# Kernel optimization log

Measured on AMD Instinct MI355X. Metric: run time of the kernel, lower is better.

Reference implementation:

```python
import jax, jax.numpy as jnp
import numpy as np

F_, E_, B_, D_, H_, O_ = 4, 8, 4096, 512, 1024, 512


def setup_inputs() -> dict:
    key = jax.random.key(0)
    ks = jax.random.split(key, 7)
    s = 0.02  # small init scale to keep activations sane
    return {
        "features": jax.random.normal(ks[0], (F_, B_, D_), jnp.float32),
        "W1": jax.random.normal(ks[1], (F_, E_, D_, H_), jnp.float32) * s,
        "b1": jax.random.normal(ks[2], (F_, E_, H_), jnp.float32) * s,
        "W2": jax.random.normal(ks[3], (F_, E_, H_, O_), jnp.float32) * s,
        "b2": jax.random.normal(ks[4], (F_, E_, O_), jnp.float32) * s,
        "Wg": jax.random.normal(ks[5], (F_, D_, E_), jnp.float32) * s,
        "bg": jax.random.normal(ks[6], (F_, E_), jnp.float32) * s,
    }


def reference(features, W1, b1, W2, b2, Wg, bg):
    # Gate: softmax over experts, per feature. [F,B,E]
    gate = jax.nn.softmax(jnp.einsum('fbd,fde->fbe', features, Wg) + bg[:, None, :], axis=-1)
    # All experts computed densely (soft MoE): hidden [F,B,E,H]
    h = jax.nn.relu(jnp.einsum('fbd,fedh->fbeh', features, W1) + b1[:, None, :, :])
    # Expert outputs [F,B,E,O]
    eo = jnp.einsum('fbeh,feho->fbeo', h, W2) + b2[:, None, :, :]
    # Gate-weighted sum over experts, then mean over features -> [B,O]
    weighted = jnp.einsum('fbe,fbeo->fbo', gate, eo)
    return jnp.mean(weighted, axis=0)
```

## Files before the change

kernel.cpp:

```cpp
#include <hip/hip_runtime.h>


#define F_ 4
#define E_ 8
#define B_ 4096
#define D_ 512
#define H_ 1024
#define O_ 512

typedef unsigned short ushort_t;
typedef __bf16 bf16x8 __attribute__((ext_vector_type(8)));
typedef float f32x4 __attribute__((ext_vector_type(4)));
typedef unsigned short ushort8_t __attribute__((ext_vector_type(8)));

__device__ inline ushort_t f2bf(float f) {
  union { float f; unsigned u; } v; v.f = f;
  unsigned r = v.u + 0x7FFFu + ((v.u >> 16) & 1u);
  return (ushort_t)(r >> 16);
}
__device__ inline float bf2f(ushort_t u) {
  union { unsigned u; float f; } v; v.u = ((unsigned)u) << 16;
  return v.f;
}

__device__ inline void async16(const void* g, void* l) {
  __builtin_amdgcn_global_load_lds(
      (const __attribute__((address_space(1))) unsigned int*)g,
      (__attribute__((address_space(3))) unsigned int*)l, 16, 0, 0);
}

__device__ inline unsigned ldsOff(const void* p) {
  return (unsigned)(unsigned long long)(const __attribute__((address_space(3))) char*)p;
}
__device__ inline bf16x8 dsr128(unsigned byteOff) {
  bf16x8 r;
  asm volatile("ds_read_b128 %0, %1" : "=v"(r) : "v"(byteOff));
  return r;
}

__global__ void prep_kernel(const float* __restrict__ features, const float* __restrict__ Wg,
                            const float* __restrict__ bg, float* __restrict__ g2,
                            ushort_t* __restrict__ featbf) {
  const int fb = blockIdx.x;
  const int f = fb >> 12, b = fb & (B_ - 1);
  const int lane = threadIdx.x;
  const float* feat = features + ((size_t)f * B_ + b) * D_;
  const float* wg = Wg + (size_t)f * D_ * E_;
  const int d0 = lane * 8;
  float ff[8];
  *(float4*)&ff[0] = *(const float4*)&feat[d0];
  *(float4*)&ff[4] = *(const float4*)&feat[d0 + 4];
  ushort8_t u;
#pragma unroll
  for (int k = 0; k < 8; ++k) u[k] = f2bf(ff[k]);
  *(ushort8_t*)&featbf[((size_t)f * B_ + b) * D_ + d0] = u;

  float acc[E_] = {0.f, 0.f, 0.f, 0.f, 0.f, 0.f, 0.f, 0.f};
#pragma unroll
  for (int k = 0; k < 8; ++k) {
    const float fv = ff[k];
    const float4 w0 = ((const float4*)(wg + (size_t)(d0 + k) * E_))[0];
    const float4 w1 = ((const float4*)(wg + (size_t)(d0 + k) * E_))[1];
    acc[0] += fv * w0.x; acc[1] += fv * w0.y; acc[2] += fv * w0.z; acc[3] += fv * w0.w;
    acc[4] += fv * w1.x; acc[5] += fv * w1.y; acc[6] += fv * w1.z; acc[7] += fv * w1.w;
  }
#pragma unroll
  for (int off = 32; off >= 1; off >>= 1)
#pragma unroll
    for (int e = 0; e < E_; ++e) acc[e] += __shfl_xor(acc[e], off, 64);
  float lg[E_], mx = -1e30f;
#pragma unroll
  for (int e = 0; e < E_; ++e) { lg[e] = acc[e] + bg[f * E_ + e]; mx = fmaxf(mx, lg[e]); }
  float s = 0.f;
#pragma unroll
  for (int e = 0; e < E_; ++e) { lg[e] = __expf(lg[e] - mx); s += lg[e]; }
  const float inv = 1.f / (s * (float)F_);
  if (lane < E_) g2[((size_t)f * B_ + b) * E_ + lane] = lg[lane] * inv;
}

__global__ void transpose_cast_kernel(const float* __restrict__ in, ushort_t* __restrict__ out,
                                      int R, int C) {
  __shared__ float tile[64][65];
  const size_t zoff = (size_t)blockIdx.z * R * C;
  in += zoff; out += zoff;
  const int tx = threadIdx.x & 63, ty = threadIdx.x >> 6;
  const int r0 = blockIdx.y * 64, c0 = blockIdx.x * 64;
#pragma unroll
  for (int i = 0; i < 16; ++i) {
    const int r = ty + i * 4;
    tile[r][tx] = in[(size_t)(r0 + r) * C + c0 + tx];
  }
  __syncthreads();
#pragma unroll
  for (int i = 0; i < 16; ++i) {
    const int c = ty + i * 4;
    out[(size_t)(c0 + c) * R + r0 + tx] = f2bf(tile[tx][c]);
  }
}


#define FSW(r) (((r) + ((r) >> 2)) & 3)

#define VM8 asm volatile("s_waitcnt vmcnt(8)" ::: "memory")
#define VM4 asm volatile("s_waitcnt vmcnt(4)" ::: "memory")
#define VM0 asm volatile("s_waitcnt vmcnt(0)" ::: "memory")
#define VMN ((void)0)

#define G1_STAGE(ktn, SLOT) { \
    ushort_t* s_ = &lds[(SLOT) * 8192]; \
    const ushort_t* a_ = aG + (ktn) * 32; \
    const ushort_t* b_ = bG + (ktn) * 32; \
    async16(a_,           s_ + t * 8); \
    async16(a_ + 64 * D_, s_ + 2048 + t * 8); \
    async16(b_,           s_ + 4096 + t * 8); \
    async16(b_ + 64 * D_, s_ + 6144 + t * 8); }

#define G2_STAGE(ktn, SLOT) { \
    ushort_t* s_ = &lds[(SLOT) * 8192]; \
    const ushort_t* a_ = HfA + (size_t)((ktn) >> 5) * ((size_t)B_ * H_) + aOff + ((ktn) & 31) * 32; \
    const ushort_t* b_ = w2A + (size_t)((ktn) >> 5) * ((size_t)O_ * H_) + bOff + ((ktn) & 31) * 32; \
    async16(a_,           s_ + t * 8); \
    async16(a_ + 64 * H_, s_ + 2048 + t * 8); \
    async16(b_,           s_ + 4096 + t * 8); \
    async16(b_ + 64 * H_, s_ + 6144 + t * 8); }

#define GSTEP(kt, SLOT, STG, VMS, STAGEM) { \
    const unsigned sb = ldsB + (SLOT) * 16384u; \
    bf16x8 af[4], bfr[4]; \
    _Pragma("unroll") for (int i_ = 0; i_ < 4; ++i_) af[i_] = dsr128(sb + aRd + i_ * 1024u); \
    _Pragma("unroll") for (int j_ = 0; j_ < 4; ++j_) bfr[j_] = dsr128(sb + bRd + j_ * 1024u); \
    asm volatile("s_waitcnt lgkmcnt(0)" ::: "memory"); \
    __builtin_amdgcn_sched_barrier(0); \
    __builtin_amdgcn_s_setprio(1); \
    _Pragma("unroll") for (int i_ = 0; i_ < 4; ++i_) \
      _Pragma("unroll") for (int j_ = 0; j_ < 4; ++j_) \
        acc[i_][j_] = __builtin_amdgcn_mfma_f32_16x16x32_bf16(bfr[j_], af[i_], acc[i_][j_], 0, 0, 0); \
    __builtin_amdgcn_s_setprio(0); \
    __builtin_amdgcn_sched_barrier(0); \
    __builtin_amdgcn_s_barrier(); \
    if (STG) { STAGEM((kt) + 3, SLOT); } \
    VMS; \
    __builtin_amdgcn_s_barrier(); \
    __builtin_amdgcn_sched_barrier(0); }

__global__ __launch_bounds__(256, 3) void gemm1_kernel(
    const ushort_t* __restrict__ featbf, const ushort_t* __restrict__ w1t,
    const float* __restrict__ b1, const float* __restrict__ g2,
    ushort_t* __restrict__ Hf, int f) {
  __shared__ __align__(16) ushort_t lds[24576];
  const int id = blockIdx.x;
  const int e = id & 7;
  const int s = id >> 3;
  const int n0 = (s & 7) * 128;
  const int m0 = (s >> 3) * 128;
  const ushort_t* A  = featbf + (size_t)f * B_ * D_;
  const ushort_t* Bp = w1t + ((size_t)f * E_ + e) * (size_t)H_ * D_;
  const float* b1e = b1 + ((size_t)f * E_ + e) * H_;
  const float* g2f = g2 + (size_t)f * B_ * E_;
  ushort_t* HfE = Hf + (size_t)e * B_ * H_;

  const int t = threadIdx.x, lane = t & 63, w = t >> 6;
  const int wm = w & 1, wn = w >> 1;
  const int lr = lane & 15, q = lane >> 4;
  const unsigned ldsB = ldsOff(lds);
  const unsigned caBy = (unsigned)((q ^ FSW(lr)) * 16);
  const unsigned aRd = (unsigned)((wm * 64 + lr) * 64) + caBy;
  const unsigned bRd = 8192u + (unsigned)((wn * 64 + lr) * 64) + caBy;

  const int rr = t >> 2;
  const int cc = (t & 3) ^ FSW(rr);
  const ushort_t* aG = A  + (size_t)(m0 + rr) * D_ + cc * 8;
  const ushort_t* bG = Bp + (size_t)(n0 + rr) * D_ + cc * 8;

  f32x4 acc[4][4];
#pragma unroll
  for (int i = 0; i < 4; ++i)
#pragma unroll
    for (int j = 0; j < 4; ++j) acc[i][j] = (f32x4){0.f, 0.f, 0.f, 0.f};

  G1_STAGE(0, 0); G1_STAGE(1, 1); G1_STAGE(2, 2);
  VM8;
  __builtin_amdgcn_s_barrier();
  __builtin_amdgcn_sched_barrier(0);

  for (int b = 0; b < 12; b += 3) {
    GSTEP(b + 0, 0, 1, VM8, G1_STAGE);
    GSTEP(b + 1, 1, 1, VM8, G1_STAGE);
    GSTEP(b + 2, 2, 1, VM8, G1_STAGE);
  }
  GSTEP(12, 0, 1, VM8, G1_STAGE);
  GSTEP(13, 1, 0, VM4, G1_STAGE);
  GSTEP(14, 2, 0, VM0, G1_STAGE);
  GSTEP(15, 0, 0, VMN, G1_STAGE);

  ushort_t* cb = lds;
#pragma unroll
  for (int i = 0; i < 4; ++i) {
    const int ml = wm * 64 + i * 16 + lr;
    const float gv = g2f[(size_t)(m0 + ml) * E_ + e];
#pragma unroll
    for (int j = 0; j < 4; ++j) {
      const int nl = wn * 64 + j * 16 + q * 4;
      const float4 bb = *(const float4*)&b1e[n0 + nl];
      ushort4 o;
      o.x = f2bf(fmaxf(acc[i][j][0] + bb.x, 0.f) * gv);
      o.y = f2bf(fmaxf(acc[i][j][1] + bb.y, 0.f) * gv);
      o.z = f2bf(fmaxf(acc[i][j][2] + bb.z, 0.f) * gv);
      o.w = f2bf(fmaxf(acc[i][j][3] + bb.w, 0.f) * gv);
      *(ushort4*)&cb[ml * 136 + nl] = o;
    }
  }
  __syncthreads();
  const int row = t >> 1, half = t & 1;
  const ushort_t* src = &cb[row * 136 + half * 64];
  ushort_t* dst = HfE + (size_t)(m0 + row) * H_ + n0 + half * 64;
#pragma unroll
  for (int c = 0; c < 8; ++c)
    *(ushort8_t*)(dst + c * 8) = *(const ushort8_t*)(src + c * 8);
}

__global__ __launch_bounds__(256, 3) void gemm2_kernel(
    const ushort_t* __restrict__ Hf, const ushort_t* __restrict__ w2t,
    const float* __restrict__ b2, const float* __restrict__ g2,
    ushort_t* __restrict__ part, int f) {
  __shared__ __align__(16) ushort_t lds[24576];
  const int id = blockIdx.x;
  const int grp = id & 3;
  const int s = id >> 2;
  const int n0 = (s & 3) * 128;
  const int m0 = (s >> 2) * 128;
  const int e0 = grp * 2;
  const ushort_t* HfA = Hf + (size_t)e0 * B_ * H_;
  const ushort_t* w2A = w2t + ((size_t)f * E_ + e0) * (size_t)O_ * H_;
  const float* g2f = g2 + (size_t)f * B_ * E_;

  const int t = threadIdx.x, lane = t & 63, w = t >> 6;
  const int wm = w & 1, wn = w >> 1;
  const int lr = lane & 15, q = lane >> 4;
  const unsigned ldsB = ldsOff(lds);
  const unsigned caBy = (unsigned)((q ^ FSW(lr)) * 16);
  const unsigned aRd = (unsigned)((wm * 64 + lr) * 64) + caBy;
  const unsigned bRd = 8192u + (unsigned)((wn * 64 + lr) * 64) + caBy;

  const int rr = t >> 2;
  const int cc = (t & 3) ^ FSW(rr);
  const size_t aOff = (size_t)(m0 + rr) * H_ + cc * 8;
  const size_t bOff = (size_t)(n0 + rr) * H_ + cc * 8;

  f32x4 acc[4][4];
#pragma unroll
  for (int i = 0; i < 4; ++i)
#pragma unroll
    for (int j = 0; j < 4; ++j) acc[i][j] = (f32x4){0.f, 0.f, 0.f, 0.f};

  G2_STAGE(0, 0); G2_STAGE(1, 1); G2_STAGE(2, 2);
  VM8;
  __builtin_amdgcn_s_barrier();
  __builtin_amdgcn_sched_barrier(0);

  for (int b = 0; b < 60; b += 3) {
    GSTEP(b + 0, 0, 1, VM8, G2_STAGE);
    GSTEP(b + 1, 1, 1, VM8, G2_STAGE);
    GSTEP(b + 2, 2, 1, VM8, G2_STAGE);
  }
  GSTEP(60, 0, 1, VM8, G2_STAGE);
  GSTEP(61, 1, 0, VM4, G2_STAGE);
  GSTEP(62, 2, 0, VM0, G2_STAGE);
  GSTEP(63, 0, 0, VMN, G2_STAGE);

  ushort_t* cb = lds;
  const float* b2e0 = b2 + ((size_t)f * E_ + e0) * O_;
  const float* b2e1 = b2e0 + O_;
#pragma unroll
  for (int i = 0; i < 4; ++i) {
    const int ml = wm * 64 + i * 16 + lr;
    const float gv0 = g2f[(size_t)(m0 + ml) * E_ + e0];
    const float gv1 = g2f[(size_t)(m0 + ml) * E_ + e0 + 1];
#pragma unroll
    for (int j = 0; j < 4; ++j) {
      const int nl = wn * 64 + j * 16 + q * 4;
      const int n = n0 + nl;
      const float4 c0 = *(const float4*)&b2e0[n];
      const float4 c1 = *(const float4*)&b2e1[n];
      ushort4 o;
      o.x = f2bf(acc[i][j][0] + gv0 * c0.x + gv1 * c1.x);
      o.y = f2bf(acc[i][j][1] + gv0 * c0.y + gv1 * c1.y);
      o.z = f2bf(acc[i][j][2] + gv0 * c0.z + gv1 * c1.z);
      o.w = f2bf(acc[i][j][3] + gv0 * c0.w + gv1 * c1.w);
      *(ushort4*)&cb[ml * 136 + nl] = o;
    }
  }
  __syncthreads();
  const int row = t >> 1, half = t & 1;
  const ushort_t* src = &cb[row * 136 + half * 64];
  ushort_t* dst = part + (size_t)(f * 4 + grp) * (B_ * O_) + (size_t)(m0 + row) * O_ + n0 + half * 64;
#pragma unroll
  for (int c = 0; c < 8; ++c)
    *(ushort8_t*)(dst + c * 8) = *(const ushort8_t*)(src + c * 8);
}

__global__ void reduce_kernel(const ushort_t* __restrict__ part, float* __restrict__ out) {
  const size_t p = ((size_t)blockIdx.x * 256 + threadIdx.x) * 8;
  float s[8] = {0.f, 0.f, 0.f, 0.f, 0.f, 0.f, 0.f, 0.f};
#pragma unroll
  for (int k = 0; k < F_ * 4; ++k) {
    const ushort8_t u = *(const ushort8_t*)&part[(size_t)k * (B_ * O_) + p];
#pragma unroll
    for (int j = 0; j < 8; ++j) s[j] += bf2f(u[j]);
  }
  float4 o0 = {s[0], s[1], s[2], s[3]}, o1 = {s[4], s[5], s[6], s[7]};
  *(float4*)&out[p] = o0;
  *(float4*)&out[p + 4] = o1;
}

extern "C" void kernel_launch(void* const* d_in, const int* in_sizes, int n_in,
                              void* d_out, int out_size, void* d_ws, size_t ws_size,
                              hipStream_t stream) {
  const float* features = (const float*)d_in[0];
  const float* W1 = (const float*)d_in[1];
  const float* b1 = (const float*)d_in[2];
  const float* W2 = (const float*)d_in[3];
  const float* b2 = (const float*)d_in[4];
  const float* Wg = (const float*)d_in[5];
  const float* bg = (const float*)d_in[6];
  float* out = (float*)d_out;

  char* ws = (char*)d_ws;
  ushort_t* featbf = (ushort_t*)ws;
  ushort_t* w1t    = (ushort_t*)(ws + 16777216);
  ushort_t* w2t    = (ushort_t*)(ws + 50331648);
  float*    g2     = (float*)(ws + 83886080);
  ushort_t* Hf     = (ushort_t*)(ws + 84410368);
  ushort_t* part   = (ushort_t*)(ws + 151519232);

  prep_kernel<<<F_ * B_, 64, 0, stream>>>(features, Wg, bg, g2, featbf);
  transpose_cast_kernel<<<dim3(H_ / 64, D_ / 64, F_ * E_), 256, 0, stream>>>(W1, w1t, D_, H_);
  transpose_cast_kernel<<<dim3(O_ / 64, H_ / 64, F_ * E_), 256, 0, stream>>>(W2, w2t, H_, O_);

  for (int f = 0; f < F_; ++f) {
    gemm1_kernel<<<2048, 256, 0, stream>>>(featbf, w1t, b1, g2, Hf, f);
    gemm2_kernel<<<512, 256, 0, stream>>>(Hf, w2t, b2, g2, part, f);
  }
  reduce_kernel<<<B_ * O_ / 8 / 256, 256, 0, stream>>>(part, out);
}
```

Before: 657.9 us.

## Enlarge GEMM tiles to 256x256/128x256 with 512-thread blocks and BK=64

```diff
diff --git a/kernel.cpp b/kernel.cpp
--- a/kernel.cpp
+++ b/kernel.cpp
@@ -37,6 +37,11 @@
   asm volatile("ds_read_b128 %0, %1" : "=v"(r) : "v"(byteOff));
   return r;
 }
+
+#define VM0 asm volatile("s_waitcnt vmcnt(0)" ::: "memory")
+#define VM6 asm volatile("s_waitcnt vmcnt(6)" ::: "memory")
+#define BAR { __builtin_amdgcn_sched_barrier(0); __builtin_amdgcn_s_barrier(); \
+              __builtin_amdgcn_sched_barrier(0); }
 
 __global__ void prep_kernel(const float* __restrict__ features, const float* __restrict__ Wg,
                             const float* __restrict__ bg, float* __restrict__ g2,
@@ -99,36 +104,129 @@
 }
 
 
-#define FSW(r) (((r) + ((r) >> 2)) & 3)
-
-#define VM8 asm volatile("s_waitcnt vmcnt(8)" ::: "memory")
-#define VM4 asm volatile("s_waitcnt vmcnt(4)" ::: "memory")
-#define VM0 asm volatile("s_waitcnt vmcnt(0)" ::: "memory")
-#define VMN ((void)0)
-
-#define G1_STAGE(ktn, SLOT) { \
-    ushort_t* s_ = &lds[(SLOT) * 8192]; \
-    const ushort_t* a_ = aG + (ktn) * 32; \
-    const ushort_t* b_ = bG + (ktn) * 32; \
-    async16(a_,           s_ + t * 8); \
-    async16(a_ + 64 * D_, s_ + 2048 + t * 8); \
-    async16(b_,           s_ + 4096 + t * 8); \
-    async16(b_ + 64 * D_, s_ + 6144 + t * 8); }
-
-#define G2_STAGE(ktn, SLOT) { \
-    ushort_t* s_ = &lds[(SLOT) * 8192]; \
-    const ushort_t* a_ = HfA + (size_t)((ktn) >> 5) * ((size_t)B_ * H_) + aOff + ((ktn) & 31) * 32; \
-    const ushort_t* b_ = w2A + (size_t)((ktn) >> 5) * ((size_t)O_ * H_) + bOff + ((ktn) & 31) * 32; \
-    async16(a_,           s_ + t * 8); \
-    async16(a_ + 64 * H_, s_ + 2048 + t * 8); \
-    async16(b_,           s_ + 4096 + t * 8); \
-    async16(b_ + 64 * H_, s_ + 6144 + t * 8); }
-
-#define GSTEP(kt, SLOT, STG, VMS, STAGEM) { \
-    const unsigned sb = ldsB + (SLOT) * 16384u; \
+#define G1_STAGE(ktn, c) { \
+    ushort_t* s_ = &lds[(c) * 32768]; \
+    const ushort_t* a_ = aG + (ktn) * 64; \
+    const ushort_t* b_ = bG + (ktn) * 64; \
+    _Pragma("unroll") for (int p = 0; p < 4; ++p) { \
+      async16(a_ + (size_t)p * (64 * D_), s_ + p * 4096 + t * 8); \
+      async16(b_ + (size_t)p * (64 * D_), s_ + 16384 + p * 4096 + t * 8); } }
+
+#define G1_PHASE(sb, kh) { \
+    bf16x8 af[8], bfr[4]; \
+    const unsigned cx = (unsigned)((((kh) * 4 + q) ^ (lr & 7)) * 16); \
+    _Pragma("unroll") for (int i_ = 0; i_ < 8; ++i_) \
+      af[i_] = dsr128((sb) + (unsigned)((wm * 128 + i_ * 16 + lr) * 128) + cx); \
+    _Pragma("unroll") for (int j_ = 0; j_ < 4; ++j_) \
+      bfr[j_] = dsr128((sb) + 32768u + (unsigned)((wn * 64 + j_ * 16 + lr) * 128) + cx); \
+    asm volatile("s_waitcnt lgkmcnt(0)" ::: "memory"); \
+    __builtin_amdgcn_sched_barrier(0); \
+    __builtin_amdgcn_s_setprio(1); \
+    _Pragma("unroll") for (int i_ = 0; i_ < 8; ++i_) \
+      _Pragma("unroll") for (int j_ = 0; j_ < 4; ++j_) \
+        acc[i_][j_] = __builtin_amdgcn_mfma_f32_16x16x32_bf16(bfr[j_], af[i_], acc[i_][j_], 0, 0, 0); \
+    __builtin_amdgcn_s_setprio(0); \
+    __builtin_amdgcn_sched_barrier(0); }
+
+#define G1_ITER(kt, c) { \
+    const unsigned sb = ldsB + (c) * 65536u; \
+    G1_STAGE((kt) + 1, (c) ^ 1); \
+    G1_PHASE(sb, 0); \
+    G1_PHASE(sb, 1); \
+    VM0; BAR; }
+
+__global__ __launch_bounds__(512, 2) void gemm1_kernel(
+    const ushort_t* __restrict__ featbf, const ushort_t* __restrict__ w1t,
+    const float* __restrict__ b1, const float* __restrict__ g2,
+    ushort_t* __restrict__ Hf, int f) {
+  __shared__ __align__(16) ushort_t lds[65536];
+  const int id = blockIdx.x;
+  const int e = id & 7;
+  const int s = id >> 3;
+  const int n0 = (s & 3) * 256;
+  const int m0 = (s >> 2) * 256;
+  const ushort_t* A  = featbf + (size_t)f * B_ * D_;
+  const ushort_t* Bp = w1t + ((size_t)f * E_ + e) * (size_t)H_ * D_;
+  const float* b1e = b1 + ((size_t)f * E_ + e) * H_;
+  const float* g2f = g2 + (size_t)f * B_ * E_;
+  ushort_t* HfE = Hf + (size_t)e * B_ * H_;
+
+  const int t = threadIdx.x, lane = t & 63, w = t >> 6;
+  const int wm = w >> 2, wn = w & 3;
+  const int lr = lane & 15, q = lane >> 4;
+  const unsigned ldsB = ldsOff(lds);
+
+  const int rr = t >> 3;
+  const int cc = (t & 7) ^ (rr & 7);
+  const ushort_t* aG = A  + (size_t)(m0 + rr) * D_ + cc * 8;
+  const ushort_t* bG = Bp + (size_t)(n0 + rr) * D_ + cc * 8;
+
+  f32x4 acc[8][4];
+#pragma unroll
+  for (int i = 0; i < 8; ++i)
+#pragma unroll
+    for (int j = 0; j < 4; ++j) acc[i][j] = (f32x4){0.f, 0.f, 0.f, 0.f};
+
+  G1_STAGE(0, 0);
+  VM0; BAR;
+
+  G1_ITER(0, 0); G1_ITER(1, 1);
+  G1_ITER(2, 0); G1_ITER(3, 1);
+  G1_ITER(4, 0); G1_ITER(5, 1);
+  G1_ITER(6, 0);
+  { const unsigned sb = ldsB + 65536u;
+    G1_PHASE(sb, 0); G1_PHASE(sb, 1); }
+
+  __syncthreads();
+  ushort_t* cb = lds;
+#pragma unroll
+  for (int mh = 0; mh < 2; ++mh) {
+    if (wm == mh) {
+#pragma unroll
+      for (int i = 0; i < 8; ++i) {
+        const int rl = i * 16 + lr;
+        const float gv = g2f[(size_t)(m0 + mh * 128 + rl) * E_ + e];
+#pragma unroll
+        for (int j = 0; j < 4; ++j) {
+          const int nl = wn * 64 + j * 16 + q * 4;
+          const float4 bb = *(const float4*)&b1e[n0 + nl];
+          ushort4 o;
+          o.x = f2bf(fmaxf(acc[i][j][0] + bb.x, 0.f) * gv);
+          o.y = f2bf(fmaxf(acc[i][j][1] + bb.y, 0.f) * gv);
+          o.z = f2bf(fmaxf(acc[i][j][2] + bb.z, 0.f) * gv);
+          o.w = f2bf(fmaxf(acc[i][j][3] + bb.w, 0.f) * gv);
+          *(ushort4*)&cb[rl * 264 + nl] = o;
+        }
+      }
+    }
+    __syncthreads();
+    const int row = t >> 2, seg = t & 3;
+    const ushort_t* src = &cb[row * 264 + seg * 64];
+    ushort_t* dst = HfE + (size_t)(m0 + mh * 128 + row) * H_ + n0 + seg * 64;
+#pragma unroll
+    for (int c2 = 0; c2 < 8; ++c2)
+      *(ushort8_t*)(dst + c2 * 8) = *(const ushort8_t*)(src + c2 * 8);
+    __syncthreads();
+  }
+}
+
+
+#define G2_STAGE(ktn, c) { \
+    ushort_t* s_ = &lds2[(c) * 24576]; \
+    const ushort_t* a_ = Hf + (size_t)(e0 + ((ktn) >> 4)) * ((size_t)B_ * H_) + aOff + ((ktn) & 15) * 64; \
+    const ushort_t* b_ = w2tF + (size_t)(e0 + ((ktn) >> 4)) * ((size_t)O_ * H_) + bOff + ((ktn) & 15) * 64; \
+    _Pragma("unroll") for (int p = 0; p < 2; ++p) \
+      async16(a_ + (size_t)p * (64 * H_), s_ + p * 4096 + t * 8); \
+    _Pragma("unroll") for (int p = 0; p < 4; ++p) \
+      async16(b_ + (size_t)p * (64 * H_), s_ + 8192 + p * 4096 + t * 8); }
+
+#define G2_PHASE(sb, kh) { \
     bf16x8 af[4], bfr[4]; \
-    _Pragma("unroll") for (int i_ = 0; i_ < 4; ++i_) af[i_] = dsr128(sb + aRd + i_ * 1024u); \
-    _Pragma("unroll") for (int j_ = 0; j_ < 4; ++j_) bfr[j_] = dsr128(sb + bRd + j_ * 1024u); \
+    const unsigned cx = (unsigned)((((kh) * 4 + q) ^ (lr & 7)) * 16); \
+    _Pragma("unroll") for (int i_ = 0; i_ < 4; ++i_) \
+      af[i_] = dsr128((sb) + (unsigned)((wm * 64 + i_ * 16 + lr) * 128) + cx); \
+    _Pragma("unroll") for (int j_ = 0; j_ < 4; ++j_) \
+      bfr[j_] = dsr128((sb) + 16384u + (unsigned)((wn * 64 + j_ * 16 + lr) * 128) + cx); \
     asm volatile("s_waitcnt lgkmcnt(0)" ::: "memory"); \
     __builtin_amdgcn_sched_barrier(0); \
     __builtin_amdgcn_s_setprio(1); \
@@ -136,114 +234,36 @@
       _Pragma("unroll") for (int j_ = 0; j_ < 4; ++j_) \
         acc[i_][j_] = __builtin_amdgcn_mfma_f32_16x16x32_bf16(bfr[j_], af[i_], acc[i_][j_], 0, 0, 0); \
     __builtin_amdgcn_s_setprio(0); \
-    __builtin_amdgcn_sched_barrier(0); \
-    __builtin_amdgcn_s_barrier(); \
-    if (STG) { STAGEM((kt) + 3, SLOT); } \
-    VMS; \
-    __builtin_amdgcn_s_barrier(); \
     __builtin_amdgcn_sched_barrier(0); }
 
-__global__ __launch_bounds__(256, 3) void gemm1_kernel(
-    const ushort_t* __restrict__ featbf, const ushort_t* __restrict__ w1t,
-    const float* __restrict__ b1, const float* __restrict__ g2,
-    ushort_t* __restrict__ Hf, int f) {
-  __shared__ __align__(16) ushort_t lds[24576];
-  const int id = blockIdx.x;
-  const int e = id & 7;
-  const int s = id >> 3;
-  const int n0 = (s & 7) * 128;
-  const int m0 = (s >> 3) * 128;
-  const ushort_t* A  = featbf + (size_t)f * B_ * D_;
-  const ushort_t* Bp = w1t + ((size_t)f * E_ + e) * (size_t)H_ * D_;
-  const float* b1e = b1 + ((size_t)f * E_ + e) * H_;
-  const float* g2f = g2 + (size_t)f * B_ * E_;
-  ushort_t* HfE = Hf + (size_t)e * B_ * H_;
-
-  const int t = threadIdx.x, lane = t & 63, w = t >> 6;
-  const int wm = w & 1, wn = w >> 1;
-  const int lr = lane & 15, q = lane >> 4;
-  const unsigned ldsB = ldsOff(lds);
-  const unsigned caBy = (unsigned)((q ^ FSW(lr)) * 16);
-  const unsigned aRd = (unsigned)((wm * 64 + lr) * 64) + caBy;
-  const unsigned bRd = 8192u + (unsigned)((wn * 64 + lr) * 64) + caBy;
-
-  const int rr = t >> 2;
-  const int cc = (t & 3) ^ FSW(rr);
-  const ushort_t* aG = A  + (size_t)(m0 + rr) * D_ + cc * 8;
-  const ushort_t* bG = Bp + (size_t)(n0 + rr) * D_ + cc * 8;
-
-  f32x4 acc[4][4];
-#pragma unroll
-  for (int i = 0; i < 4; ++i)
-#pragma unroll
-    for (int j = 0; j < 4; ++j) acc[i][j] = (f32x4){0.f, 0.f, 0.f, 0.f};
-
-  G1_STAGE(0, 0); G1_STAGE(1, 1); G1_STAGE(2, 2);
-  VM8;
-  __builtin_amdgcn_s_barrier();
-  __builtin_amdgcn_sched_barrier(0);
-
-  for (int b = 0; b < 12; b += 3) {
-    GSTEP(b + 0, 0, 1, VM8, G1_STAGE);
-    GSTEP(b + 1, 1, 1, VM8, G1_STAGE);
-    GSTEP(b + 2, 2, 1, VM8, G1_STAGE);
-  }
-  GSTEP(12, 0, 1, VM8, G1_STAGE);
-  GSTEP(13, 1, 0, VM4, G1_STAGE);
-  GSTEP(14, 2, 0, VM0, G1_STAGE);
-  GSTEP(15, 0, 0, VMN, G1_STAGE);
-
-  ushort_t* cb = lds;
-#pragma unroll
-  for (int i = 0; i < 4; ++i) {
-    const int ml = wm * 64 + i * 16 + lr;
-    const float gv = g2f[(size_t)(m0 + ml) * E_ + e];
-#pragma unroll
-    for (int j = 0; j < 4; ++j) {
-      const int nl = wn * 64 + j * 16 + q * 4;
-      const float4 bb = *(const float4*)&b1e[n0 + nl];
-      ushort4 o;
-      o.x = f2bf(fmaxf(acc[i][j][0] + bb.x, 0.f) * gv);
-      o.y = f2bf(fmaxf(acc[i][j][1] + bb.y, 0.f) * gv);
-      o.z = f2bf(fmaxf(acc[i][j][2] + bb.z, 0.f) * gv);
-      o.w = f2bf(fmaxf(acc[i][j][3] + bb.w, 0.f) * gv);
-      *(ushort4*)&cb[ml * 136 + nl] = o;
-    }
-  }
-  __syncthreads();
-  const int row = t >> 1, half = t & 1;
-  const ushort_t* src = &cb[row * 136 + half * 64];
-  ushort_t* dst = HfE + (size_t)(m0 + row) * H_ + n0 + half * 64;
-#pragma unroll
-  for (int c = 0; c < 8; ++c)
-    *(ushort8_t*)(dst + c * 8) = *(const ushort8_t*)(src + c * 8);
-}
-
-__global__ __launch_bounds__(256, 3) void gemm2_kernel(
+#define G2_ITER(kt, c, cn) { \
+    const unsigned sb = ldsB + (c) * 49152u; \
+    G2_STAGE((kt) + 2, cn); \
+    G2_PHASE(sb, 0); \
+    G2_PHASE(sb, 1); \
+    VM6; BAR; }
+
+__global__ __launch_bounds__(512, 2) void gemm2_kernel(
     const ushort_t* __restrict__ Hf, const ushort_t* __restrict__ w2t,
     const float* __restrict__ b2, const float* __restrict__ g2,
     ushort_t* __restrict__ part, int f) {
-  __shared__ __align__(16) ushort_t lds[24576];
+  __shared__ __align__(16) ushort_t lds2[73728];
   const int id = blockIdx.x;
   const int grp = id & 3;
   const int s = id >> 2;
-  const int n0 = (s & 3) * 128;
-  const int m0 = (s >> 2) * 128;
+  const int n0 = (s & 1) * 256;
+  const int m0 = (s >> 1) * 128;
   const int e0 = grp * 2;
-  const ushort_t* HfA = Hf + (size_t)e0 * B_ * H_;
-  const ushort_t* w2A = w2t + ((size_t)f * E_ + e0) * (size_t)O_ * H_;
+  const ushort_t* w2tF = w2t + (size_t)f * E_ * O_ * H_;
   const float* g2f = g2 + (size_t)f * B_ * E_;
 
   const int t = threadIdx.x, lane = t & 63, w = t >> 6;
-  const int wm = w & 1, wn = w >> 1;
+  const int wm = w >> 2, wn = w & 3;
   const int lr = lane & 15, q = lane >> 4;
-  const unsigned ldsB = ldsOff(lds);
-  const unsigned caBy = (unsigned)((q ^ FSW(lr)) * 16);
-  const unsigned aRd = (unsigned)((wm * 64 + lr) * 64) + caBy;
-  const unsigned bRd = 8192u + (unsigned)((wn * 64 + lr) * 64) + caBy;
-
-  const int rr = t >> 2;
-  const int cc = (t & 3) ^ FSW(rr);
+  const unsigned ldsB = ldsOff(lds2);
+
+  const int rr = t >> 3;
+  const int cc = (t & 7) ^ (rr & 7);
   const size_t aOff = (size_t)(m0 + rr) * H_ + cc * 8;
   const size_t bOff = (size_t)(n0 + rr) * H_ + cc * 8;
 
@@ -253,22 +273,21 @@
 #pragma unroll
     for (int j = 0; j < 4; ++j) acc[i][j] = (f32x4){0.f, 0.f, 0.f, 0.f};
 
-  G2_STAGE(0, 0); G2_STAGE(1, 1); G2_STAGE(2, 2);
-  VM8;
-  __builtin_amdgcn_s_barrier();
-  __builtin_amdgcn_sched_barrier(0);
-
-  for (int b = 0; b < 60; b += 3) {
-    GSTEP(b + 0, 0, 1, VM8, G2_STAGE);
-    GSTEP(b + 1, 1, 1, VM8, G2_STAGE);
-    GSTEP(b + 2, 2, 1, VM8, G2_STAGE);
-  }
-  GSTEP(60, 0, 1, VM8, G2_STAGE);
-  GSTEP(61, 1, 0, VM4, G2_STAGE);
-  GSTEP(62, 2, 0, VM0, G2_STAGE);
-  GSTEP(63, 0, 0, VMN, G2_STAGE);
-
-  ushort_t* cb = lds;
+  G2_STAGE(0, 0); G2_STAGE(1, 1);
+  VM6; BAR;
+
+  for (int b = 0; b < 30; b += 3) {
+    G2_ITER(b + 0, 0, 2);
+    G2_ITER(b + 1, 1, 0);
+    G2_ITER(b + 2, 2, 1);
+  }
+  { const unsigned sb = ldsB + 0u;
+    G2_PHASE(sb, 0); G2_PHASE(sb, 1); VM0; BAR; }
+  { const unsigned sb = ldsB + 49152u;
+    G2_PHASE(sb, 0); G2_PHASE(sb, 1); }
+
+  __syncthreads();
+  ushort_t* cb = lds2;
   const float* b2e0 = b2 + ((size_t)f * E_ + e0) * O_;
   const float* b2e1 = b2e0 + O_;
 #pragma unroll
@@ -287,16 +306,16 @@
       o.y = f2bf(acc[i][j][1] + gv0 * c0.y + gv1 * c1.y);
       o.z = f2bf(acc[i][j][2] + gv0 * c0.z + gv1 * c1.z);
       o.w = f2bf(acc[i][j][3] + gv0 * c0.w + gv1 * c1.w);
-      *(ushort4*)&cb[ml * 136 + nl] = o;
+      *(ushort4*)&cb[ml * 264 + nl] = o;
     }
   }
   __syncthreads();
-  const int row = t >> 1, half = t & 1;
-  const ushort_t* src = &cb[row * 136 + half * 64];
-  ushort_t* dst = part + (size_t)(f * 4 + grp) * (B_ * O_) + (size_t)(m0 + row) * O_ + n0 + half * 64;
-#pragma unroll
-  for (int c = 0; c < 8; ++c)
-    *(ushort8_t*)(dst + c * 8) = *(const ushort8_t*)(src + c * 8);
+  const int row = t >> 2, seg = t & 3;
+  const ushort_t* src = &cb[row * 264 + seg * 64];
+  ushort_t* dst = part + (size_t)(f * 4 + grp) * (B_ * O_) + (size_t)(m0 + row) * O_ + n0 + seg * 64;
+#pragma unroll
+  for (int c2 = 0; c2 < 8; ++c2)
+    *(ushort8_t*)(dst + c2 * 8) = *(const ushort8_t*)(src + c2 * 8);
 }
 
 __global__ void reduce_kernel(const ushort_t* __restrict__ part, float* __restrict__ out) {
@@ -338,8 +357,8 @@
   transpose_cast_kernel<<<dim3(O_ / 64, H_ / 64, F_ * E_), 256, 0, stream>>>(W2, w2t, H_, O_);
 
   for (int f = 0; f < F_; ++f) {
-    gemm1_kernel<<<2048, 256, 0, stream>>>(featbf, w1t, b1, g2, Hf, f);
-    gemm2_kernel<<<512, 256, 0, stream>>>(Hf, w2t, b2, g2, part, f);
+    gemm1_kernel<<<512, 512, 0, stream>>>(featbf, w1t, b1, g2, Hf, f);
+    gemm2_kernel<<<256, 512, 0, stream>>>(Hf, w2t, b2, g2, part, f);
   }
   reduce_kernel<<<B_ * O_ / 8 / 256, 256, 0, stream>>>(part, out);
 }
```

After: 621.6 us. 5.5% less time.

## Reuse A tiles across four experts per block and batch all features per launch

Applied to the files above, without the earlier changes.

```diff
diff --git a/kernel.cpp b/kernel.cpp
--- a/kernel.cpp
+++ b/kernel.cpp
@@ -12,6 +12,7 @@
 typedef __bf16 bf16x8 __attribute__((ext_vector_type(8)));
 typedef float f32x4 __attribute__((ext_vector_type(4)));
 typedef unsigned short ushort8_t __attribute__((ext_vector_type(8)));
+typedef unsigned uint2_ __attribute__((ext_vector_type(2)));
 
 __device__ inline ushort_t f2bf(float f) {
   union { float f; unsigned u; } v; v.f = f;
@@ -37,6 +38,18 @@
   asm volatile("ds_read_b128 %0, %1" : "=v"(r) : "v"(byteOff));
   return r;
 }
+__device__ inline void dsw64(unsigned byteOff, uint2_ v) {
+  asm volatile("ds_write_b64 %0, %1" :: "v"(byteOff), "v"(v) : "memory");
+}
+
+#define LGKM0 asm volatile("s_waitcnt lgkmcnt(0)" ::: "memory")
+#define VM8 asm volatile("s_waitcnt vmcnt(8)" ::: "memory")
+#define VM4 asm volatile("s_waitcnt vmcnt(4)" ::: "memory")
+#define VM0 asm volatile("s_waitcnt vmcnt(0)" ::: "memory")
+#define VNONE ((void)0)
+#define SCB __builtin_amdgcn_sched_barrier(0)
+#define SBAR __builtin_amdgcn_s_barrier()
+#define EBAR { SCB; LGKM0; asm volatile("" ::: "memory"); SBAR; SCB; }
 
 __global__ void prep_kernel(const float* __restrict__ features, const float* __restrict__ Wg,
                             const float* __restrict__ bg, float* __restrict__ g2,
@@ -99,78 +112,64 @@
 }
 
 
-#define FSW(r) (((r) + ((r) >> 2)) & 3)
-
-#define VM8 asm volatile("s_waitcnt vmcnt(8)" ::: "memory")
-#define VM4 asm volatile("s_waitcnt vmcnt(4)" ::: "memory")
-#define VM0 asm volatile("s_waitcnt vmcnt(0)" ::: "memory")
-#define VMN ((void)0)
-
-#define G1_STAGE(ktn, SLOT) { \
-    ushort_t* s_ = &lds[(SLOT) * 8192]; \
-    const ushort_t* a_ = aG + (ktn) * 32; \
-    const ushort_t* b_ = bG + (ktn) * 32; \
-    async16(a_,           s_ + t * 8); \
-    async16(a_ + 64 * D_, s_ + 2048 + t * 8); \
-    async16(b_,           s_ + 4096 + t * 8); \
-    async16(b_ + 64 * D_, s_ + 6144 + t * 8); }
-
-#define G2_STAGE(ktn, SLOT) { \
-    ushort_t* s_ = &lds[(SLOT) * 8192]; \
-    const ushort_t* a_ = HfA + (size_t)((ktn) >> 5) * ((size_t)B_ * H_) + aOff + ((ktn) & 31) * 32; \
-    const ushort_t* b_ = w2A + (size_t)((ktn) >> 5) * ((size_t)O_ * H_) + bOff + ((ktn) & 31) * 32; \
-    async16(a_,           s_ + t * 8); \
-    async16(a_ + 64 * H_, s_ + 2048 + t * 8); \
-    async16(b_,           s_ + 4096 + t * 8); \
-    async16(b_ + 64 * H_, s_ + 6144 + t * 8); }
-
-#define GSTEP(kt, SLOT, STG, VMS, STAGEM) { \
-    const unsigned sb = ldsB + (SLOT) * 16384u; \
+#define KITER(STAGEEXPR, VMS) { \
+    const unsigned sb = ldsB + soff; \
     bf16x8 af[4], bfr[4]; \
     _Pragma("unroll") for (int i_ = 0; i_ < 4; ++i_) af[i_] = dsr128(sb + aRd + i_ * 1024u); \
     _Pragma("unroll") for (int j_ = 0; j_ < 4; ++j_) bfr[j_] = dsr128(sb + bRd + j_ * 1024u); \
-    asm volatile("s_waitcnt lgkmcnt(0)" ::: "memory"); \
-    __builtin_amdgcn_sched_barrier(0); \
+    LGKM0; SCB; \
     __builtin_amdgcn_s_setprio(1); \
     _Pragma("unroll") for (int i_ = 0; i_ < 4; ++i_) \
       _Pragma("unroll") for (int j_ = 0; j_ < 4; ++j_) \
         acc[i_][j_] = __builtin_amdgcn_mfma_f32_16x16x32_bf16(bfr[j_], af[i_], acc[i_][j_], 0, 0, 0); \
     __builtin_amdgcn_s_setprio(0); \
-    __builtin_amdgcn_sched_barrier(0); \
-    __builtin_amdgcn_s_barrier(); \
-    if (STG) { STAGEM((kt) + 3, SLOT); } \
+    SCB; asm volatile("" ::: "memory"); SBAR; SCB; \
+    STAGEEXPR; \
     VMS; \
-    __builtin_amdgcn_s_barrier(); \
-    __builtin_amdgcn_sched_barrier(0); }
+    asm volatile("" ::: "memory"); SBAR; SCB; \
+    ++tt; soff = (soff >= 32768u) ? 0u : (soff + 16384u); }
+
+
+#define STAGE1T(T3, SOFF) { const int t3 = (T3); \
+    const ushort_t* a_ = aG + (t3 & 15) * 32; \
+    const ushort_t* b_ = bG + (size_t)(t3 >> 4) * ((size_t)H_ * D_) + (t3 & 15) * 32; \
+    char* s_ = (char*)lds + (SOFF); \
+    async16(a_,            s_ + t * 16); \
+    async16(a_ + 64 * D_,  s_ + 4096 + t * 16); \
+    async16(b_,            s_ + 8192 + t * 16); \
+    async16(b_ + 64 * D_,  s_ + 12288 + t * 16); }
+#define STAGE1 STAGE1T(tt + 3, soff)
 
 __global__ __launch_bounds__(256, 3) void gemm1_kernel(
     const ushort_t* __restrict__ featbf, const ushort_t* __restrict__ w1t,
     const float* __restrict__ b1, const float* __restrict__ g2,
-    ushort_t* __restrict__ Hf, int f) {
-  __shared__ __align__(16) ushort_t lds[24576];
+    ushort_t* __restrict__ Hf, int fBase, size_t hfStride) {
+  __shared__ __align__(16) ushort_t lds[26752];
   const int id = blockIdx.x;
-  const int e = id & 7;
-  const int s = id >> 3;
+  const int s = id & 255;
+  const int e0 = ((id >> 8) & 1) * 4;
+  const int fi = (id >> 9) & 3;
+  const int f = fBase + fi;
   const int n0 = (s & 7) * 128;
   const int m0 = (s >> 3) * 128;
   const ushort_t* A  = featbf + (size_t)f * B_ * D_;
-  const ushort_t* Bp = w1t + ((size_t)f * E_ + e) * (size_t)H_ * D_;
-  const float* b1e = b1 + ((size_t)f * E_ + e) * H_;
   const float* g2f = g2 + (size_t)f * B_ * E_;
-  ushort_t* HfE = Hf + (size_t)e * B_ * H_;
+  ushort_t* HfF = Hf + (size_t)fi * hfStride;
 
   const int t = threadIdx.x, lane = t & 63, w = t >> 6;
   const int wm = w & 1, wn = w >> 1;
   const int lr = lane & 15, q = lane >> 4;
   const unsigned ldsB = ldsOff(lds);
-  const unsigned caBy = (unsigned)((q ^ FSW(lr)) * 16);
-  const unsigned aRd = (unsigned)((wm * 64 + lr) * 64) + caBy;
-  const unsigned bRd = 8192u + (unsigned)((wn * 64 + lr) * 64) + caBy;
+  const unsigned cRd = (unsigned)((q ^ ((lr >> 1) & 3)) << 4);
+  const unsigned aRd = (unsigned)((wm * 64 + lr) * 64) + cRd;
+  const unsigned bRd = 8192u + (unsigned)((wn * 64 + lr) * 64) + cRd;
+  const unsigned cbB = 49152u;
 
   const int rr = t >> 2;
-  const int cc = (t & 3) ^ FSW(rr);
-  const ushort_t* aG = A  + (size_t)(m0 + rr) * D_ + cc * 8;
-  const ushort_t* bG = Bp + (size_t)(n0 + rr) * D_ + cc * 8;
+  const int cc = (t & 3) ^ ((rr >> 1) & 3);
+  const ushort_t* aG = A + (size_t)(m0 + rr) * D_ + cc * 8;
+  const ushort_t* bG = w1t + ((size_t)f * E_ + e0) * ((size_t)H_ * D_) +
+                       (size_t)(n0 + rr) * D_ + cc * 8;
 
   f32x4 acc[4][4];
 #pragma unroll
@@ -178,72 +177,95 @@
 #pragma unroll
     for (int j = 0; j < 4; ++j) acc[i][j] = (f32x4){0.f, 0.f, 0.f, 0.f};
 
-  G1_STAGE(0, 0); G1_STAGE(1, 1); G1_STAGE(2, 2);
+  STAGE1T(0, 0u); STAGE1T(1, 16384u); STAGE1T(2, 32768u);
   VM8;
-  __builtin_amdgcn_s_barrier();
-  __builtin_amdgcn_sched_barrier(0);
-
-  for (int b = 0; b < 12; b += 3) {
-    GSTEP(b + 0, 0, 1, VM8, G1_STAGE);
-    GSTEP(b + 1, 1, 1, VM8, G1_STAGE);
-    GSTEP(b + 2, 2, 1, VM8, G1_STAGE);
-  }
-  GSTEP(12, 0, 1, VM8, G1_STAGE);
-  GSTEP(13, 1, 0, VM4, G1_STAGE);
-  GSTEP(14, 2, 0, VM0, G1_STAGE);
-  GSTEP(15, 0, 0, VMN, G1_STAGE);
-
-  ushort_t* cb = lds;
-#pragma unroll
-  for (int i = 0; i < 4; ++i) {
-    const int ml = wm * 64 + i * 16 + lr;
-    const float gv = g2f[(size_t)(m0 + ml) * E_ + e];
-#pragma unroll
-    for (int j = 0; j < 4; ++j) {
-      const int nl = wn * 64 + j * 16 + q * 4;
-      const float4 bb = *(const float4*)&b1e[n0 + nl];
-      ushort4 o;
-      o.x = f2bf(fmaxf(acc[i][j][0] + bb.x, 0.f) * gv);
-      o.y = f2bf(fmaxf(acc[i][j][1] + bb.y, 0.f) * gv);
-      o.z = f2bf(fmaxf(acc[i][j][2] + bb.z, 0.f) * gv);
-      o.w = f2bf(fmaxf(acc[i][j][3] + bb.w, 0.f) * gv);
-      *(ushort4*)&cb[ml * 136 + nl] = o;
-    }
-  }
-  __syncthreads();
-  const int row = t >> 1, half = t & 1;
-  const ushort_t* src = &cb[row * 136 + half * 64];
-  ushort_t* dst = HfE + (size_t)(m0 + row) * H_ + n0 + half * 64;
-#pragma unroll
-  for (int c = 0; c < 8; ++c)
-    *(ushort8_t*)(dst + c * 8) = *(const ushort8_t*)(src + c * 8);
-}
+  asm volatile("" ::: "memory"); SBAR; SCB;
+
+  int tt = 0; unsigned soff = 0;
+  for (int eg = 0; eg < 4; ++eg) {
+    if (eg < 3) {
+      for (int kk = 0; kk < 16; ++kk) KITER(STAGE1, VM8);
+    } else {
+      for (int kk = 0; kk < 13; ++kk) KITER(STAGE1, VM8);
+      KITER(VNONE, VM4);
+      KITER(VNONE, VM0);
+      KITER(VNONE, VNONE);
+    }
+    const int e = e0 + eg;
+    const float* b1e = b1 + ((size_t)f * E_ + e) * H_;
+    ushort_t* HfEe = HfF + (size_t)e * B_ * H_;
+#pragma unroll
+    for (int pr = 0; pr < 8; ++pr) {
+      if (wm == (pr >> 2)) {
+        const int I = pr & 3;
+        const float gv = g2f[(size_t)(m0 + pr * 16 + lr) * E_ + e];
+#pragma unroll
+        for (int j = 0; j < 4; ++j) {
+          const int nl = wn * 64 + j * 16 + q * 4;
+          const float4 bb = *(const float4*)&b1e[n0 + nl];
+          const unsigned p0 = (unsigned)f2bf(fmaxf(acc[I][j][0] + bb.x, 0.f) * gv) |
+                              ((unsigned)f2bf(fmaxf(acc[I][j][1] + bb.y, 0.f) * gv) << 16);
+          const unsigned p1 = (unsigned)f2bf(fmaxf(acc[I][j][2] + bb.z, 0.f) * gv) |
+                              ((unsigned)f2bf(fmaxf(acc[I][j][3] + bb.w, 0.f) * gv) << 16);
+          dsw64(cbB + (unsigned)(lr * 272 + nl * 2), (uint2_){p0, p1});
+        }
+      }
+      EBAR;
+      {
+        const int row = t >> 4, seg = t & 15;
+        const bf16x8 rv = dsr128(cbB + (unsigned)(row * 272 + seg * 16));
+        LGKM0; SCB;
+        *(ushort8_t*)(HfEe + (size_t)(m0 + pr * 16 + row) * H_ + n0 + seg * 8) =
+            __builtin_bit_cast(ushort8_t, rv);
+      }
+      EBAR;
+    }
+#pragma unroll
+    for (int i = 0; i < 4; ++i)
+#pragma unroll
+      for (int j = 0; j < 4; ++j) acc[i][j] = (f32x4){0.f, 0.f, 0.f, 0.f};
+  }
+}
+
+
+#define STAGE2T(T3, SOFF) { const int t3 = (T3); \
+    const ushort_t* a_ = HfFe + (size_t)(t3 >> 5) * ((size_t)B_ * H_) + aOff + (t3 & 31) * 32; \
+    const ushort_t* b_ = w2Fe + (size_t)(t3 >> 5) * ((size_t)O_ * H_) + bOff + (t3 & 31) * 32; \
+    char* s_ = (char*)lds + (SOFF); \
+    async16(a_,            s_ + t * 16); \
+    async16(a_ + 64 * H_,  s_ + 4096 + t * 16); \
+    async16(b_,            s_ + 8192 + t * 16); \
+    async16(b_ + 64 * H_,  s_ + 12288 + t * 16); }
+#define STAGE2 STAGE2T(tt + 3, soff)
 
 __global__ __launch_bounds__(256, 3) void gemm2_kernel(
     const ushort_t* __restrict__ Hf, const ushort_t* __restrict__ w2t,
     const float* __restrict__ b2, const float* __restrict__ g2,
-    ushort_t* __restrict__ part, int f) {
-  __shared__ __align__(16) ushort_t lds[24576];
+    ushort_t* __restrict__ part, int fBase, size_t hfStride) {
+  __shared__ __align__(16) ushort_t lds[26752];
   const int id = blockIdx.x;
-  const int grp = id & 3;
-  const int s = id >> 2;
+  const int s = id & 127;
+  const int grp = (id >> 7) & 1;
+  const int fi = (id >> 8) & 3;
+  const int f = fBase + fi;
   const int n0 = (s & 3) * 128;
   const int m0 = (s >> 2) * 128;
-  const int e0 = grp * 2;
-  const ushort_t* HfA = Hf + (size_t)e0 * B_ * H_;
-  const ushort_t* w2A = w2t + ((size_t)f * E_ + e0) * (size_t)O_ * H_;
+  const int e0 = grp * 4;
   const float* g2f = g2 + (size_t)f * B_ * E_;
+  const ushort_t* HfFe = Hf + (size_t)fi * hfStride + (size_t)e0 * B_ * H_;
+  const ushort_t* w2Fe = w2t + ((size_t)f * E_ + e0) * ((size_t)O_ * H_);
 
   const int t = threadIdx.x, lane = t & 63, w = t >> 6;
   const int wm = w & 1, wn = w >> 1;
   const int lr = lane & 15, q = lane >> 4;
   const unsigned ldsB = ldsOff(lds);
-  const unsigned caBy = (unsigned)((q ^ FSW(lr)) * 16);
-  const unsigned aRd = (unsigned)((wm * 64 + lr) * 64) + caBy;
-  const unsigned bRd = 8192u + (unsigned)((wn * 64 + lr) * 64) + caBy;
+  const unsigned cRd = (unsigned)((q ^ ((lr >> 1) & 3)) << 4);
+  const unsigned aRd = (unsigned)((wm * 64 + lr) * 64) + cRd;
+  const unsigned bRd = 8192u + (unsigned)((wn * 64 + lr) * 64) + cRd;
+  const unsigned cbB = 49152u;
 
   const int rr = t >> 2;
-  const int cc = (t & 3) ^ FSW(rr);
+  const int cc = (t & 3) ^ ((rr >> 1) & 3);
   const size_t aOff = (size_t)(m0 + rr) * H_ + cc * 8;
   const size_t bOff = (size_t)(n0 + rr) * H_ + cc * 8;
 
@@ -253,57 +275,58 @@
 #pragma unroll
     for (int j = 0; j < 4; ++j) acc[i][j] = (f32x4){0.f, 0.f, 0.f, 0.f};
 
-  G2_STAGE(0, 0); G2_STAGE(1, 1); G2_STAGE(2, 2);
+  STAGE2T(0, 0u); STAGE2T(1, 16384u); STAGE2T(2, 32768u);
   VM8;
-  __builtin_amdgcn_s_barrier();
-  __builtin_amdgcn_sched_barrier(0);
-
-  for (int b = 0; b < 60; b += 3) {
-    GSTEP(b + 0, 0, 1, VM8, G2_STAGE);
-    GSTEP(b + 1, 1, 1, VM8, G2_STAGE);
-    GSTEP(b + 2, 2, 1, VM8, G2_STAGE);
-  }
-  GSTEP(60, 0, 1, VM8, G2_STAGE);
-  GSTEP(61, 1, 0, VM4, G2_STAGE);
-  GSTEP(62, 2, 0, VM0, G2_STAGE);
-  GSTEP(63, 0, 0, VMN, G2_STAGE);
-
-  ushort_t* cb = lds;
+  asm volatile("" ::: "memory"); SBAR; SCB;
+
+  int tt = 0; unsigned soff = 0;
+  for (int kk = 0; kk < 125; ++kk) KITER(STAGE2, VM8);
+  KITER(VNONE, VM4);
+  KITER(VNONE, VM0);
+  KITER(VNONE, VNONE);
+
   const float* b2e0 = b2 + ((size_t)f * E_ + e0) * O_;
-  const float* b2e1 = b2e0 + O_;
-#pragma unroll
-  for (int i = 0; i < 4; ++i) {
-    const int ml = wm * 64 + i * 16 + lr;
-    const float gv0 = g2f[(size_t)(m0 + ml) * E_ + e0];
-    const float gv1 = g2f[(size_t)(m0 + ml) * E_ + e0 + 1];
-#pragma unroll
-    for (int j = 0; j < 4; ++j) {
-      const int nl = wn * 64 + j * 16 + q * 4;
-      const int n = n0 + nl;
-      const float4 c0 = *(const float4*)&b2e0[n];
-      const float4 c1 = *(const float4*)&b2e1[n];
-      ushort4 o;
-      o.x = f2bf(acc[i][j][0] + gv0 * c0.x + gv1 * c1.x);
-      o.y = f2bf(acc[i][j][1] + gv0 * c0.y + gv1 * c1.y);
-      o.z = f2bf(acc[i][j][2] + gv0 * c0.z + gv1 * c1.z);
-      o.w = f2bf(acc[i][j][3] + gv0 * c0.w + gv1 * c1.w);
-      *(ushort4*)&cb[ml * 136 + nl] = o;
-    }
-  }
-  __syncthreads();
-  const int row = t >> 1, half = t & 1;
-  const ushort_t* src = &cb[row * 136 + half * 64];
-  ushort_t* dst = part + (size_t)(f * 4 + grp) * (B_ * O_) + (size_t)(m0 + row) * O_ + n0 + half * 64;
-#pragma unroll
-  for (int c = 0; c < 8; ++c)
-    *(ushort8_t*)(dst + c * 8) = *(const ushort8_t*)(src + c * 8);
+  ushort_t* dstP = part + (size_t)(f * 2 + grp) * ((size_t)B_ * O_);
+#pragma unroll
+  for (int pr = 0; pr < 8; ++pr) {
+    if (wm == (pr >> 2)) {
+      const int I = pr & 3;
+      const size_t gr = (size_t)(m0 + pr * 16 + lr) * E_ + e0;
+      const float g0 = g2f[gr], g1 = g2f[gr + 1], g2v = g2f[gr + 2], g3 = g2f[gr + 3];
+#pragma unroll
+      for (int j = 0; j < 4; ++j) {
+        const int nl = wn * 64 + j * 16 + q * 4;
+        const int n = n0 + nl;
+        const float4 c0 = *(const float4*)&b2e0[n];
+        const float4 c1 = *(const float4*)&b2e0[O_ + n];
+        const float4 c2 = *(const float4*)&b2e0[2 * O_ + n];
+        const float4 c3 = *(const float4*)&b2e0[3 * O_ + n];
+        const float r0 = acc[I][j][0] + g0 * c0.x + g1 * c1.x + g2v * c2.x + g3 * c3.x;
+        const float r1 = acc[I][j][1] + g0 * c0.y + g1 * c1.y + g2v * c2.y + g3 * c3.y;
+        const float r2 = acc[I][j][2] + g0 * c0.z + g1 * c1.z + g2v * c2.z + g3 * c3.z;
+        const float r3 = acc[I][j][3] + g0 * c0.w + g1 * c1.w + g2v * c2.w + g3 * c3.w;
+        const unsigned p0 = (unsigned)f2bf(r0) | ((unsigned)f2bf(r1) << 16);
+        const unsigned p1 = (unsigned)f2bf(r2) | ((unsigned)f2bf(r3) << 16);
+        dsw64(cbB + (unsigned)(lr * 272 + nl * 2), (uint2_){p0, p1});
+      }
+    }
+    EBAR;
+    {
+      const int row = t >> 4, seg = t & 15;
+      const bf16x8 rv = dsr128(cbB + (unsigned)(row * 272 + seg * 16));
+      LGKM0; SCB;
+      *(ushort8_t*)(dstP + (size_t)(m0 + pr * 16 + row) * O_ + n0 + seg * 8) =
+          __builtin_bit_cast(ushort8_t, rv);
+    }
+    EBAR;
+  }
 }
 
 __global__ void reduce_kernel(const ushort_t* __restrict__ part, float* __restrict__ out) {
   const size_t p = ((size_t)blockIdx.x * 256 + threadIdx.x) * 8;
   float s[8] = {0.f, 0.f, 0.f, 0.f, 0.f, 0.f, 0.f, 0.f};
 #pragma unroll
-  for (int k = 0; k < F_ * 4; ++k) {
+  for (int k = 0; k < F_ * 2; ++k) {
     const ushort8_t u = *(const ushort8_t*)&part[(size_t)k * (B_ * O_) + p];
 #pragma unroll
     for (int j = 0; j < 8; ++j) s[j] += bf2f(u[j]);
@@ -331,15 +354,22 @@
   ushort_t* w2t    = (ushort_t*)(ws + 50331648);
   float*    g2     = (float*)(ws + 83886080);
   ushort_t* Hf     = (ushort_t*)(ws + 84410368);
-  ushort_t* part   = (ushort_t*)(ws + 151519232);
+  const bool big = ws_size >= (size_t)386400256;
+  ushort_t* part   = big ? (ushort_t*)(ws + 352845824)
+                         : (ushort_t*)(ws + 151519232);
 
   prep_kernel<<<F_ * B_, 64, 0, stream>>>(features, Wg, bg, g2, featbf);
   transpose_cast_kernel<<<dim3(H_ / 64, D_ / 64, F_ * E_), 256, 0, stream>>>(W1, w1t, D_, H_);
   transpose_cast_kernel<<<dim3(O_ / 64, H_ / 64, F_ * E_), 256, 0, stream>>>(W2, w2t, H_, O_);
 
-  for (int f = 0; f < F_; ++f) {
-    gemm1_kernel<<<2048, 256, 0, stream>>>(featbf, w1t, b1, g2, Hf, f);
-    gemm2_kernel<<<512, 256, 0, stream>>>(Hf, w2t, b2, g2, part, f);
+  if (big) {
+    gemm1_kernel<<<2048, 256, 0, stream>>>(featbf, w1t, b1, g2, Hf, 0, (size_t)E_ * B_ * H_);
+    gemm2_kernel<<<1024, 256, 0, stream>>>(Hf, w2t, b2, g2, part, 0, (size_t)E_ * B_ * H_);
+  } else {
+    for (int f = 0; f < F_; ++f) {
+      gemm1_kernel<<<512, 256, 0, stream>>>(featbf, w1t, b1, g2, Hf, f, 0);
+      gemm2_kernel<<<256, 256, 0, stream>>>(Hf, w2t, b2, g2, part, f, 0);
+    }
   }
   reduce_kernel<<<B_ * O_ / 8 / 256, 256, 0, stream>>>(part, out);
 }
```

Result: slower. 882.5 us (+34.2%).
